# Performance work log

Measured on AMD Instinct MI355X. Metric: run time of the kernel, lower is better.

## Reference

```python
import jax, jax.numpy as jnp
import numpy as np

H = 16          # num_attention_heads
SCALE = (1024.0 / 16.0) ** 0.5  # attention_head_size = hidden/num_hidden_layers
EPS = 1e-12
NEG = -jnp.inf


def layer_norm(x, g, b):
    mu = jnp.mean(x, axis=-1, keepdims=True)
    var = jnp.mean((x - mu) ** 2, axis=-1, keepdims=True)
    return (x - mu) * jax.lax.rsqrt(var + EPS) * g + b


def setup_inputs() -> dict:
    key = jax.random.key(0)
    ks = jax.random.split(key, 8)
    B, S, D, F = 4, 2048, 1024, 4096
    s = 0.02
    return {
        "hidden_state": jax.random.normal(ks[0], (B, S, D), jnp.float32),
        "attention_mask": jnp.ones((B, S), jnp.int32),
        "Wq": jax.random.normal(ks[1], (D, D), jnp.float32) * s,
        "Wk": jax.random.normal(ks[2], (D, D), jnp.float32) * s,
        "Wv": jax.random.normal(ks[3], (D, D), jnp.float32) * s,
        "Wo": jax.random.normal(ks[4], (D, D), jnp.float32) * s,
        "ln1_g": jnp.ones((D,), jnp.float32),
        "ln1_b": jnp.zeros((D,), jnp.float32),
        "W1": jax.random.normal(ks[5], (D, F), jnp.float32) * s,
        "b1": jnp.zeros((F,), jnp.float32),
        "W2": jax.random.normal(ks[6], (F, D), jnp.float32) * s,
        "b2": jnp.zeros((D,), jnp.float32),
        "ln2_g": jnp.ones((D,), jnp.float32),
        "ln2_b": jnp.zeros((D,), jnp.float32),
    }


def reference(hidden_state, attention_mask, Wq, Wk, Wv, Wo, ln1_g, ln1_b,
              W1, b1, W2, b2, ln2_g, ln2_b):
    B, S, D = hidden_state.shape
    # --- square attention mask (is_not_pad == 1) + causal ---
    amb = attention_mask == 1                              # [B,S] bool
    pair = amb[:, :, None] & amb[:, None, :]               # [B,S,S]
    self_mask = jnp.where(pair, 0.0, NEG)[:, None, :, :]   # [B,1,S,S]
    causal = jnp.where(jnp.triu(jnp.ones((S, S), bool), 1), NEG, 0.0)
    self_mask = self_mask + causal                         # [B,1,S,S]

    # --- self attention (pre-norm) ---
    residual = hidden_state
    x = layer_norm(hidden_state, ln1_g, ln1_b)
    q = (x @ Wq).reshape(B, S, H, D // H)
    k = (x @ Wk).reshape(B, S, H, D // H)
    v = (x @ Wv).reshape(B, S, H, D // H)
    scores = jnp.einsum('bqhd,bkhd->bhqk', q, k) / SCALE + self_mask
    probs = jax.nn.softmax(scores, axis=-1)                # dropout p=0
    ctx = jnp.einsum('bhqk,bkhd->bqhd', probs, v).reshape(B, S, D)
    x = ctx @ Wo + residual

    # --- feed forward (pre-norm, SiLU) ---
    residual = x
    y = layer_norm(x, ln2_g, ln2_b)
    y = jax.nn.silu(y @ W1 + b1) @ W2 + b2
    return y + residual
```

## Files before the change

### kernel.cpp

```cpp
#include <hip/hip_runtime.h>
#include <math.h>

typedef __attribute__((ext_vector_type(8))) short short8;
typedef __attribute__((ext_vector_type(4))) float floatx4;
typedef __attribute__((ext_vector_type(2))) unsigned int uintx2;

__device__ __forceinline__ float b2f(ushort u) {
    union { uint i; float f; } c; c.i = ((uint)u) << 16; return c.f;
}
__device__ __forceinline__ ushort f2b(float f) {
    union { float f; uint i; } c; c.f = f;
    return (ushort)((c.i + 0x7fffu + ((c.i >> 16) & 1u)) >> 16);
}

__device__ __forceinline__ void async_cp16(const ushort* g, ushort* l) {
    __builtin_amdgcn_global_load_lds(
        (const __attribute__((address_space(1))) void*)g,
        (__attribute__((address_space(3))) void*)l, 16, 0, 0);
}

__device__ __forceinline__ uint lds_u32(const void* p) {
    return (uint)(uintptr_t)(const __attribute__((address_space(3))) void*)p;
}

__device__ __forceinline__ float dpp_max16(float x) {
    int y;
    y = __builtin_amdgcn_update_dpp(__float_as_int(x), __float_as_int(x), 0xB1, 0xF, 0xF, false);
    x = fmaxf(x, __int_as_float(y));
    y = __builtin_amdgcn_update_dpp(__float_as_int(x), __float_as_int(x), 0x4E, 0xF, 0xF, false);
    x = fmaxf(x, __int_as_float(y));
    y = __builtin_amdgcn_update_dpp(__float_as_int(x), __float_as_int(x), 0x141, 0xF, 0xF, false);
    x = fmaxf(x, __int_as_float(y));
    y = __builtin_amdgcn_update_dpp(__float_as_int(x), __float_as_int(x), 0x140, 0xF, 0xF, false);
    x = fmaxf(x, __int_as_float(y));
    return x;
}

__global__ __launch_bounds__(256) void cvt_t_kernel(
    const float* __restrict__ S, ushort* __restrict__ D, int K, int N)
{
    __shared__ float ls[32][33];
    const int k0 = blockIdx.y * 32, n0 = blockIdx.x * 32;
    const int t = threadIdx.x;
    const int kr = t >> 3, nc = (t & 7) * 4;
    float4 f = *(const float4*)(S + (size_t)(k0 + kr) * N + n0 + nc);
    ls[kr][nc] = f.x; ls[kr][nc + 1] = f.y; ls[kr][nc + 2] = f.z; ls[kr][nc + 3] = f.w;
    __syncthreads();
    const int nr = t >> 3, kc = (t & 7) * 4;
    ushort4 o;
    o.x = f2b(ls[kc][nr]); o.y = f2b(ls[kc + 1][nr]);
    o.z = f2b(ls[kc + 2][nr]); o.w = f2b(ls[kc + 3][nr]);
    *(ushort4*)(D + (size_t)(n0 + nr) * K + k0 + kc) = o;
}

__global__ __launch_bounds__(256) void ln_kernel(
    const float* __restrict__ X, const float* __restrict__ G,
    const float* __restrict__ Bb, ushort* __restrict__ Y)
{
    const int row = blockIdx.x;
    const int t = threadIdx.x;
    const float* xr = X + (size_t)row * 1024;
    float4 p = ((const float4*)xr)[t];
    float s = p.x + p.y + p.z + p.w;
    float s2 = p.x * p.x + p.y * p.y + p.z * p.z + p.w * p.w;
    #pragma unroll
    for (int off = 32; off > 0; off >>= 1) {
        s += __shfl_down(s, off);
        s2 += __shfl_down(s2, off);
    }
    __shared__ float rs1[4], rs2[4];
    if ((t & 63) == 0) { rs1[t >> 6] = s; rs2[t >> 6] = s2; }
    __syncthreads();
    float S1 = rs1[0] + rs1[1] + rs1[2] + rs1[3];
    float S2 = rs2[0] + rs2[1] + rs2[2] + rs2[3];
    float mu = S1 * (1.0f / 1024.0f);
    float var = S2 * (1.0f / 1024.0f) - mu * mu;
    float rstd = rsqrtf(var + 1e-12f);
    float4 gp = ((const float4*)G)[t];
    float4 bp = ((const float4*)Bb)[t];
    ushort4 o;
    o.x = f2b((p.x - mu) * rstd * gp.x + bp.x);
    o.y = f2b((p.y - mu) * rstd * gp.y + bp.y);
    o.z = f2b((p.z - mu) * rstd * gp.z + bp.z);
    o.w = f2b((p.w - mu) * rstd * gp.w + bp.w);
    ((ushort4*)(Y + (size_t)row * 1024))[t] = o;
}

template<int BN, bool BIAS, bool SILU, bool RESID, bool OUTF32>
__global__ __launch_bounds__(256) void gemm_bt_kernel(
    const ushort* __restrict__ A, const ushort* __restrict__ Bt,
    const float* __restrict__ bias, const float* __restrict__ resid,
    void* __restrict__ Cm, int M, int N, int K)
{
    constexpr int NF = BN / 32;
    constexpr int BI = BN / 64;
    __shared__ __align__(16) ushort lsA[128 * 64];
    __shared__ __align__(16) ushort lsB[BN * 64];

    const int t = threadIdx.x;
    const int L = blockIdx.x + gridDim.x * blockIdx.y;
    const int cpx = (gridDim.x * gridDim.y) >> 3;
    const int wg = (L & 7) * cpx + (L >> 3);
    const int m0 = (wg / gridDim.x) * 128;
    const int n0 = (wg % gridDim.x) * BN;
    const int w = t >> 6;
    const int lane = t & 63;
    const int wm = (w >> 1) * 64;
    const int wn = (w & 1) * (BN / 2);
    const int quad = lane >> 4;
    const int l16 = lane & 15;

    const int lrow = lane >> 3;
    const int scol = ((lane & 7) ^ lrow) * 8;
    const ushort* gA = A + (size_t)(m0 + w * 32 + lrow) * K + scol;
    const ushort* gB = Bt + (size_t)(n0 + ((BI == 2) ? w * 32 : w * 16) + lrow) * K + scol;
    const int sw = l16 & 7;

    floatx4 acc[4][NF];
    #pragma unroll
    for (int i = 0; i < 4; ++i)
        #pragma unroll
        for (int j = 0; j < NF; ++j)
            acc[i][j] = (floatx4){0.f, 0.f, 0.f, 0.f};

    for (int k0 = 0; k0 < K; k0 += 64) {
        __syncthreads();
        #pragma unroll
        for (int i = 0; i < 4; ++i)
            async_cp16(gA + k0 + (size_t)(8 * i) * K, &lsA[(w * 32 + 8 * i) * 64]);
        if constexpr (BI == 2) {
            #pragma unroll
            for (int i = 0; i < 4; ++i)
                async_cp16(gB + k0 + (size_t)(8 * i) * K, &lsB[(w * 32 + 8 * i) * 64]);
        } else {
            #pragma unroll
            for (int i = 0; i < 2; ++i)
                async_cp16(gB + k0 + (size_t)(8 * i) * K, &lsB[(w * 16 + 8 * i) * 64]);
        }
        __syncthreads();

        #pragma unroll
        for (int h = 0; h < 2; ++h) {
            const int co = (((h << 2) | quad) ^ sw) * 8;
            short8 af[4], bf[NF];
            #pragma unroll
            for (int i = 0; i < 4; ++i)
                af[i] = *(const short8*)&lsA[(wm + i * 16 + l16) * 64 + co];
            #pragma unroll
            for (int j = 0; j < NF; ++j)
                bf[j] = *(const short8*)&lsB[(wn + j * 16 + l16) * 64 + co];
            #pragma unroll
            for (int i = 0; i < 4; ++i)
                #pragma unroll
                for (int j = 0; j < NF; ++j)
                    acc[i][j] = __builtin_amdgcn_mfma_f32_16x16x32_bf16(
                        af[i], bf[j], acc[i][j], 0, 0, 0);
        }
    }

    #pragma unroll
    for (int tn = 0; tn < NF; ++tn) {
        const int n = n0 + wn + tn * 16 + l16;
        const float bv = BIAS ? bias[n] : 0.0f;
        #pragma unroll
        for (int tm = 0; tm < 4; ++tm) {
            const int mbase = m0 + wm + tm * 16 + quad * 4;
            #pragma unroll
            for (int rr = 0; rr < 4; ++rr) {
                float v = acc[tm][tn][rr] + bv;
                if (SILU) v = v / (1.0f + __expf(-v));
                const size_t off = (size_t)(mbase + rr) * N + n;
                if (RESID) v += resid[off];
                if constexpr (OUTF32) ((float*)Cm)[off] = v;
                else                  ((ushort*)Cm)[off] = f2b(v);
            }
        }
    }
}

__global__ __launch_bounds__(256, 4) void attn_kernel(
    const ushort* __restrict__ Qm, const ushort* __restrict__ Km,
    const ushort* __restrict__ Vm, const int* __restrict__ amask,
    ushort* __restrict__ Om, int rs)
{
    __shared__ __align__(16) ushort lsQP[64][72];
    __shared__ __align__(16) ushort lsK[64][72];
    __shared__ __align__(16) ushort lsVt[64][72];
    __shared__ int lsMk[64];

    const int L = blockIdx.x + (int)(gridDim.x * blockIdx.y);
    const int bh = L & 63;
    const int pr = L >> 6;
    const int b = bh >> 4, h = bh & 15;
    const int t = threadIdx.x;
    const int w = t >> 6, lane = t & 63;
    const int quad = lane >> 4, l16 = lane & 15;

    const size_t base = ((size_t)b * 2048) * rs + (size_t)h * 64;
    const size_t obase = ((size_t)b * 2048) * 1024 + (size_t)h * 64;

    const int krow = t >> 3, kc8 = (t & 7) << 3;
    const int vp = t & 31, vc8 = (t >> 5) << 3;
    const float scale2 = 0.125f * 1.44269504f;

    ushort* strip = &lsQP[w * 16][0];
    const uint strip_a = lds_u32(strip);
    char* wp_base = (char*)strip + l16 * 32 + quad * 8;
    const uint rp = strip_a + quad * 256 + l16 * 8;

    short8 ones8;
    #pragma unroll
    for (int i = 0; i < 8; ++i) ones8[i] = (short)0x3F80;

    #pragma unroll 1
    for (int half = 0; half < 2; ++half) {
        const int qt = half ? pr : (31 - pr);
        const int q0 = qt * 64;

        __syncthreads();
        #pragma unroll
        for (int it = 0; it < 2; ++it) {
            int idx = it * 256 + t;
            int row = idx >> 3, c8 = (idx & 7) << 3;
            *(int4*)&lsQP[row][c8] =
                *(const int4*)(Qm + base + (size_t)(q0 + row) * rs + c8);
        }
        __syncthreads();

        short8 aq0 = *(const short8*)&lsQP[w * 16 + l16][quad * 8];
        short8 aq1 = *(const short8*)&lsQP[w * 16 + l16][32 + quad * 8];

        floatx4 Oacc[4];
        #pragma unroll
        for (int d = 0; d < 4; ++d) Oacc[d] = (floatx4){0.f, 0.f, 0.f, 0.f};
        floatx4 Lacc = (floatx4){0.f, 0.f, 0.f, 0.f};
        float m_i[4] = {-INFINITY, -INFINITY, -INFINITY, -INFINITY};

        int4 kr0 = *(const int4*)(Km + base + (size_t)krow * rs + kc8);
        int4 kr1 = *(const int4*)(Km + base + (size_t)(32 + krow) * rs + kc8);
        int4 vr0 = *(const int4*)(Vm + base + (size_t)(2 * vp) * rs + vc8);
        int4 vr1 = *(const int4*)(Vm + base + (size_t)(2 * vp + 1) * rs + vc8);
        int mr = amask[b * 2048 + (t & 63)];

        for (int kt = 0; kt <= qt; ++kt) {
            __syncthreads();
            *(int4*)&lsK[krow][kc8] = kr0;
            *(int4*)&lsK[32 + krow][kc8] = kr1;
            {
                const ushort* p0 = (const ushort*)&vr0;
                const ushort* p1 = (const ushort*)&vr1;
                #pragma unroll
                for (int i = 0; i < 8; ++i) {
                    uint pk = (uint)p0[i] | ((uint)p1[i] << 16);
                    *(uint*)&lsVt[vc8 + i][2 * vp] = pk;
                }
            }
            if (t < 64) lsMk[t] = mr;
            __syncthreads();

            if (kt < qt) {
                const int kn = (kt + 1) * 64;
                kr0 = *(const int4*)(Km + base + (size_t)(kn + krow) * rs + kc8);
                kr1 = *(const int4*)(Km + base + (size_t)(kn + 32 + krow) * rs + kc8);
                vr0 = *(const int4*)(Vm + base + (size_t)(kn + 2 * vp) * rs + vc8);
                vr1 = *(const int4*)(Vm + base + (size_t)(kn + 2 * vp + 1) * rs + vc8);
                mr = amask[b * 2048 + kn + (t & 63)];
            }

            floatx4 sa[4];
            #pragma unroll
            for (int j = 0; j < 4; ++j) {
                short8 bk0 = *(const short8*)&lsK[j * 16 + l16][quad * 8];
                short8 bk1 = *(const short8*)&lsK[j * 16 + l16][32 + quad * 8];
                floatx4 z = (floatx4){0.f, 0.f, 0.f, 0.f};
                z = __builtin_amdgcn_mfma_f32_16x16x32_bf16(aq0, bk0, z, 0, 0, 0);
                sa[j] = __builtin_amdgcn_mfma_f32_16x16x32_bf16(aq1, bk1, z, 0, 0, 0);
            }

            float kb[4];
            #pragma unroll
            for (int j = 0; j < 4; ++j)
                kb[j] = (lsMk[j * 16 + l16] == 1) ? 0.f : -INFINITY;
            const bool diag = (kt == qt);

            float sv[4][4];
            float mxl[4];
            #pragma unroll
            for (int rr = 0; rr < 4; ++rr) {
                const int qrow = w * 16 + quad * 4 + rr;
                float mxv = -INFINITY;
                #pragma unroll
                for (int j = 0; j < 4; ++j) {
                    float v = sa[j][rr] * scale2 + kb[j];
                    if (diag) v = (j * 16 + l16 <= qrow) ? v : -INFINITY;
                    sv[rr][j] = v;
                    mxv = fmaxf(mxv, v);
                }
                mxl[rr] = mxv;
            }
            int grow = (mxl[0] > m_i[0] + 8.0f) | (mxl[1] > m_i[1] + 8.0f) |
                       (mxl[2] > m_i[2] + 8.0f) | (mxl[3] > m_i[3] + 8.0f);
            if (__any(grow)) {
                #pragma unroll
                for (int rr = 0; rr < 4; ++rr) {
                    const float mx = dpp_max16(mxl[rr]);
                    const float m_new = fmaxf(m_i[rr], mx);
                    const float al = exp2f(m_i[rr] - m_new);
                    m_i[rr] = m_new;
                    #pragma unroll
                    for (int d = 0; d < 4; ++d) Oacc[d][rr] *= al;
                    Lacc[rr] *= al;
                }
            }

            #pragma unroll
            for (int j = 0; j < 4; ++j) {
                float p0 = exp2f(sv[0][j] - m_i[0]);
                float p1 = exp2f(sv[1][j] - m_i[1]);
                float p2 = exp2f(sv[2][j] - m_i[2]);
                float p3 = exp2f(sv[3][j] - m_i[3]);
                uint w0, w1;
                asm("v_cvt_pk_bf16_f32 %0, %1, %2" : "=v"(w0) : "v"(p0), "v"(p1));
                asm("v_cvt_pk_bf16_f32 %0, %1, %2" : "=v"(w1) : "v"(p2), "v"(p3));
                *(uint2*)(wp_base + j * 512) = make_uint2(w0, w1);
            }

            asm volatile("s_waitcnt lgkmcnt(0)" ::: "memory");
            uintx2 t0, t1, t2, t3;
            asm volatile("ds_read_b64_tr_b16 %0, %1 offset:0"    : "=v"(t0) : "v"(rp));
            asm volatile("ds_read_b64_tr_b16 %0, %1 offset:128"  : "=v"(t1) : "v"(rp));
            asm volatile("ds_read_b64_tr_b16 %0, %1 offset:1024" : "=v"(t2) : "v"(rp));
            asm volatile("ds_read_b64_tr_b16 %0, %1 offset:1152" : "=v"(t3) : "v"(rp));
            asm volatile("s_waitcnt lgkmcnt(0)" ::: "memory");
            __builtin_amdgcn_sched_barrier(0);
            union { short8 s; uint u[4]; } ua0, ua1;
            ua0.u[0] = t0.x; ua0.u[1] = t0.y; ua0.u[2] = t1.x; ua0.u[3] = t1.y;
            ua1.u[0] = t2.x; ua1.u[1] = t2.y; ua1.u[2] = t3.x; ua1.u[3] = t3.y;
            const short8 ap0 = ua0.s;
            const short8 ap1 = ua1.s;

            #pragma unroll
            for (int d = 0; d < 4; ++d) {
                short8 bv0 = *(const short8*)&lsVt[d * 16 + l16][quad * 8];
                short8 bv1 = *(const short8*)&lsVt[d * 16 + l16][32 + quad * 8];
                Oacc[d] = __builtin_amdgcn_mfma_f32_16x16x32_bf16(ap0, bv0, Oacc[d], 0, 0, 0);
                Oacc[d] = __builtin_amdgcn_mfma_f32_16x16x32_bf16(ap1, bv1, Oacc[d], 0, 0, 0);
            }
            Lacc = __builtin_amdgcn_mfma_f32_16x16x32_bf16(ap0, ones8, Lacc, 0, 0, 0);
            Lacc = __builtin_amdgcn_mfma_f32_16x16x32_bf16(ap1, ones8, Lacc, 0, 0, 0);
        }

        #pragma unroll
        for (int rr = 0; rr < 4; ++rr) {
            const float inv = 1.0f / Lacc[rr];
            const int row = q0 + w * 16 + quad * 4 + rr;
            ushort* op = Om + obase + (size_t)row * 1024;
            #pragma unroll
            for (int d = 0; d < 4; ++d)
                op[d * 16 + l16] = f2b(Oacc[d][rr] * inv);
        }
    }
}

extern "C" void kernel_launch(void* const* d_in, const int* in_sizes, int n_in,
                              void* d_out, int out_size, void* d_ws, size_t ws_size,
                              hipStream_t stream) {
    const float* hidden = (const float*)d_in[0];
    const int*   amask  = (const int*)d_in[1];
    const float* Wq  = (const float*)d_in[2];
    const float* Wk  = (const float*)d_in[3];
    const float* Wv  = (const float*)d_in[4];
    const float* Wo  = (const float*)d_in[5];
    const float* l1g = (const float*)d_in[6];
    const float* l1b = (const float*)d_in[7];
    const float* W1  = (const float*)d_in[8];
    const float* b1  = (const float*)d_in[9];
    const float* W2  = (const float*)d_in[10];
    const float* b2  = (const float*)d_in[11];
    const float* l2g = (const float*)d_in[12];
    const float* l2b = (const float*)d_in[13];

    const int M = 8192;
    const size_t MB = 1048576;
    char* ws = (char*)d_ws;
    ushort* xa    = (ushort*)(ws);
    ushort* qkvb  = (ushort*)(ws + 16 * MB);
    ushort* Wqkvt = (ushort*)(ws + 64 * MB);
    ushort* Wot   = (ushort*)(ws + 70 * MB);
    ushort* W1t   = (ushort*)(ws);
    ushort* W2t   = (ushort*)(ws + 8 * MB);
    ushort* yb    = (ushort*)(ws + 16 * MB);
    ushort* hbc   = (ushort*)(ws + 32 * MB);
    float*  x2    = (float*)d_out;

    cvt_t_kernel<<<dim3(32, 32), 256, 0, stream>>>(Wq, Wqkvt, 1024, 1024);
    cvt_t_kernel<<<dim3(32, 32), 256, 0, stream>>>(Wk, Wqkvt + (size_t)1024 * 1024, 1024, 1024);
    cvt_t_kernel<<<dim3(32, 32), 256, 0, stream>>>(Wv, Wqkvt + (size_t)2048 * 1024, 1024, 1024);
    cvt_t_kernel<<<dim3(32, 32), 256, 0, stream>>>(Wo, Wot, 1024, 1024);

    ln_kernel<<<M, 256, 0, stream>>>(hidden, l1g, l1b, xa);
    gemm_bt_kernel<128, false, false, false, false><<<dim3(24, 64), 256, 0, stream>>>(
        xa, Wqkvt, nullptr, nullptr, qkvb, M, 3072, 1024);
    attn_kernel<<<dim3(16, 64), 256, 0, stream>>>(
        qkvb, qkvb + 1024, qkvb + 2048, amask, xa, 3072);
    gemm_bt_kernel<64, false, false, true, true><<<dim3(16, 64), 256, 0, stream>>>(
        xa, Wot, nullptr, hidden, x2, M, 1024, 1024);

    cvt_t_kernel<<<dim3(128, 32), 256, 0, stream>>>(W1, W1t, 1024, 4096);
    cvt_t_kernel<<<dim3(32, 128), 256, 0, stream>>>(W2, W2t, 4096, 1024);

    ln_kernel<<<M, 256, 0, stream>>>(x2, l2g, l2b, yb);
    for (int mc = 0; mc < 2; ++mc) {
        const size_t off = (size_t)mc * 4096 * 1024;
        gemm_bt_kernel<128, true, true, false, false><<<dim3(32, 32), 256, 0, stream>>>(
            yb + off, W1t, b1, nullptr, hbc, 4096, 4096, 1024);
        gemm_bt_kernel<64, true, false, true, true><<<dim3(16, 32), 256, 0, stream>>>(
            hbc, W2t, b2, x2 + off, (void*)(x2 + off), 4096, 1024, 4096);
    }
}
```

Measured before the change: 587.7 us.

## Load V tiles via async global-to-LDS copies and transpose-read with ds_read_tr

Replaces the register-staged V load plus manual scalar transpose into LDS with direct global_load_lds async copies into a double-buffered V tile. The PV matmul operands are then fetched with ds_read_b64_tr_b16 transpose reads. This removes the per-iteration 32-bit LDS scatter stores and VGPRs used to stage V, and lets V loading overlap compute. The cost is more LDS (two 8KB buffers), explicit waits on transpose reads per d-block, and reliance on the implicit completion ordering of async copies across barriers.

```diff
diff --git a/kernel.cpp b/kernel.cpp
--- a/kernel.cpp
+++ b/kernel.cpp
@@ -185,7 +185,7 @@
 {
     __shared__ __align__(16) ushort lsQP[64][72];
     __shared__ __align__(16) ushort lsK[64][72];
-    __shared__ __align__(16) ushort lsVt[64][72];
+    __shared__ __align__(16) ushort lsV2[2][4096];
     __shared__ int lsMk[64];
 
     const int L = blockIdx.x + (int)(gridDim.x * blockIdx.y);
@@ -200,8 +200,10 @@
     const size_t obase = ((size_t)b * 2048) * 1024 + (size_t)h * 64;
 
     const int krow = t >> 3, kc8 = (t & 7) << 3;
-    const int vp = t & 31, vc8 = (t >> 5) << 3;
     const float scale2 = 0.125f * 1.44269504f;
+
+    const int vkofs = ((lane >> 5) << 2) + ((lane >> 1) & 3);
+    const int vdofs = ((lane >> 3) & 3) * 16 + (lane & 1) * 8;
 
     ushort* strip = &lsQP[w * 16][0];
     const uint strip_a = lds_u32(strip);
@@ -218,6 +220,12 @@
         const int q0 = qt * 64;
 
         __syncthreads();
+
+        async_cp16(Vm + base + (size_t)(16 * w + vkofs) * rs + vdofs,
+                   &lsV2[0][(4 * w) * 256]);
+        async_cp16(Vm + base + (size_t)(16 * w + 8 + vkofs) * rs + vdofs,
+                   &lsV2[0][(4 * w + 2) * 256]);
+
         #pragma unroll
         for (int it = 0; it < 2; ++it) {
             int idx = it * 256 + t;
@@ -238,23 +246,12 @@
 
         int4 kr0 = *(const int4*)(Km + base + (size_t)krow * rs + kc8);
         int4 kr1 = *(const int4*)(Km + base + (size_t)(32 + krow) * rs + kc8);
-        int4 vr0 = *(const int4*)(Vm + base + (size_t)(2 * vp) * rs + vc8);
-        int4 vr1 = *(const int4*)(Vm + base + (size_t)(2 * vp + 1) * rs + vc8);
         int mr = amask[b * 2048 + (t & 63)];
 
         for (int kt = 0; kt <= qt; ++kt) {
             __syncthreads();
             *(int4*)&lsK[krow][kc8] = kr0;
             *(int4*)&lsK[32 + krow][kc8] = kr1;
-            {
-                const ushort* p0 = (const ushort*)&vr0;
-                const ushort* p1 = (const ushort*)&vr1;
-                #pragma unroll
-                for (int i = 0; i < 8; ++i) {
-                    uint pk = (uint)p0[i] | ((uint)p1[i] << 16);
-                    *(uint*)&lsVt[vc8 + i][2 * vp] = pk;
-                }
-            }
             if (t < 64) lsMk[t] = mr;
             __syncthreads();
 
@@ -262,9 +259,12 @@
                 const int kn = (kt + 1) * 64;
                 kr0 = *(const int4*)(Km + base + (size_t)(kn + krow) * rs + kc8);
                 kr1 = *(const int4*)(Km + base + (size_t)(kn + 32 + krow) * rs + kc8);
-                vr0 = *(const int4*)(Vm + base + (size_t)(kn + 2 * vp) * rs + vc8);
-                vr1 = *(const int4*)(Vm + base + (size_t)(kn + 2 * vp + 1) * rs + vc8);
                 mr = amask[b * 2048 + kn + (t & 63)];
+                ushort* vd = &lsV2[(kt + 1) & 1][0];
+                async_cp16(Vm + base + (size_t)(kn + 16 * w + vkofs) * rs + vdofs,
+                           vd + (4 * w) * 256);
+                async_cp16(Vm + base + (size_t)(kn + 16 * w + 8 + vkofs) * rs + vdofs,
+                           vd + (4 * w + 2) * 256);
             }
 
             floatx4 sa[4];
@@ -339,12 +339,22 @@
             const short8 ap0 = ua0.s;
             const short8 ap1 = ua1.s;
 
-            #pragma unroll
-            for (int d = 0; d < 4; ++d) {
-                short8 bv0 = *(const short8*)&lsVt[d * 16 + l16][quad * 8];
-                short8 bv1 = *(const short8*)&lsVt[d * 16 + l16][32 + quad * 8];
-                Oacc[d] = __builtin_amdgcn_mfma_f32_16x16x32_bf16(ap0, bv0, Oacc[d], 0, 0, 0);
-                Oacc[d] = __builtin_amdgcn_mfma_f32_16x16x32_bf16(ap1, bv1, Oacc[d], 0, 0, 0);
+            const uint vb = lds_u32(&lsV2[kt & 1][0]) + quad * 1024 + l16 * 8;
+            #pragma unroll
+            for (int db = 0; db < 4; ++db) {
+                const uint vbd = vb + db * 128;
+                uintx2 v0, v1, v2, v3;
+                asm volatile("ds_read_b64_tr_b16 %0, %1 offset:0"    : "=v"(v0) : "v"(vbd));
+                asm volatile("ds_read_b64_tr_b16 %0, %1 offset:512"  : "=v"(v1) : "v"(vbd));
+                asm volatile("ds_read_b64_tr_b16 %0, %1 offset:4096" : "=v"(v2) : "v"(vbd));
+                asm volatile("ds_read_b64_tr_b16 %0, %1 offset:4608" : "=v"(v3) : "v"(vbd));
+                asm volatile("s_waitcnt lgkmcnt(0)" ::: "memory");
+                __builtin_amdgcn_sched_barrier(0);
+                union { short8 s; uint u[4]; } ub0, ub1;
+                ub0.u[0] = v0.x; ub0.u[1] = v0.y; ub0.u[2] = v1.x; ub0.u[3] = v1.y;
+                ub1.u[0] = v2.x; ub1.u[1] = v2.y; ub1.u[2] = v3.x; ub1.u[3] = v3.y;
+                Oacc[db] = __builtin_amdgcn_mfma_f32_16x16x32_bf16(ap0, ub0.s, Oacc[db], 0, 0, 0);
+                Oacc[db] = __builtin_amdgcn_mfma_f32_16x16x32_bf16(ap1, ub1.s, Oacc[db], 0, 0, 0);
             }
             Lacc = __builtin_amdgcn_mfma_f32_16x16x32_bf16(ap0, ones8, Lacc, 0, 0, 0);
             Lacc = __builtin_amdgcn_mfma_f32_16x16x32_bf16(ap1, ones8, Lacc, 0, 0, 0);
```

After: 573.6 us. 1.02x faster.
